# Kernel tuning notes

Hardware: AMD Instinct MI355X
Metric: run time of the kernel (lower is better)

## Reference

```python
import jax, jax.numpy as jnp
import numpy as np

N, K, F, A = 20000, 32, 256, 128
BN_EPS = 1e-3  # Keras BatchNormalization default epsilon


def setup_inputs() -> dict:
    key = jax.random.key(0)
    k1, k2, k3, k4 = jax.random.split(key, 4)
    self_feats = jax.random.normal(k1, (N, F), dtype=jnp.float32)
    neigh_feats = jax.random.normal(k2, (N, K, F), dtype=jnp.float32)
    W_shared = jax.random.normal(k3, (F, A), dtype=jnp.float32) * (1.0 / np.sqrt(F))
    b_shared = jnp.zeros((A,), dtype=jnp.float32)
    gamma = jnp.ones((A,), dtype=jnp.float32)
    beta = jnp.zeros((A,), dtype=jnp.float32)
    W_out = jax.random.normal(k4, (2 * A, 1), dtype=jnp.float32) * (1.0 / np.sqrt(2 * A))
    b_out = jnp.zeros((1,), dtype=jnp.float32)
    return {"self_feats": self_feats, "neigh_feats": neigh_feats,
            "W_shared": W_shared, "b_shared": b_shared,
            "gamma": gamma, "beta": beta, "W_out": W_out, "b_out": b_out}


def _bn_train(x, gamma, beta):
    # BatchNorm in training mode: batch statistics over leading axis
    mean = jnp.mean(x, axis=0, keepdims=True)
    var = jnp.var(x, axis=0, keepdims=True)
    return (x - mean) * jax.lax.rsqrt(var + BN_EPS) * gamma + beta


def reference(self_feats, neigh_feats, W_shared, b_shared, gamma, beta, W_out, b_out):
    # shared Dense + BN on self features: [N, A]
    s = _bn_train(self_feats @ W_shared + b_shared, gamma, beta)
    # shared Dense on neighbor features, BN over flattened [N*K, A] batch
    n = neigh_feats.reshape(-1, F) @ W_shared + b_shared  # [N*K, A]
    n = _bn_train(n, gamma, beta).reshape(neigh_feats.shape[0], neigh_feats.shape[1], -1)  # [N, K, A]
    # broadcast self feats over neighbors and concat: [N, K, 2A]
    s_b = jnp.broadcast_to(s[:, None, :], n.shape)
    concat = jnp.concatenate([s_b, n], axis=2)
    # attention logits: Dense(2A -> 1), activation, softmax over neighbors
    logits = concat @ W_out + b_out  # [N, K, 1]
    logits = jax.nn.relu(logits)
    coeff = jax.nn.softmax(jnp.squeeze(logits, axis=2), axis=-1)  # [N, K]
    return coeff[:, :, None]  # [N, K, 1]
```

## Files before the change

kernel.cpp:

```cpp
#include <hip/hip_runtime.h>
#include <cstdint>
#include <cstddef>


typedef __attribute__((ext_vector_type(8))) short short8;
typedef __attribute__((ext_vector_type(4))) float float4v;

__device__ __forceinline__ unsigned short f2bf(float f) {
  union { float f; unsigned u; } v; v.f = f;
  unsigned r = v.u + 0x7FFFu + ((v.u >> 16) & 1u);
  return (unsigned short)(r >> 16);
}
__device__ __forceinline__ float bfu(unsigned v) {
  union { unsigned u; float f; } t; t.u = v << 16; return t.f;
}
__device__ __forceinline__ unsigned pkbf(float x, float y) {
  return (unsigned)f2bf(x) | ((unsigned)f2bf(y) << 16);
}

__global__ __launch_bounds__(256) void transpose_w(const float* __restrict__ W,
                                                   unsigned short* __restrict__ Wt) {
  const int n = blockIdx.x;
  const int k = threadIdx.x;
  Wt[n * 256 + k] = f2bf(W[k * 128 + n]);
}

#define BROW 264

template <bool GUARD>
__global__ __launch_bounds__(256) void stats_gemm2(
    const float* __restrict__ X, int R, int nTiles,
    const unsigned short* __restrict__ Wt,
    unsigned short* __restrict__ U,
    float* __restrict__ partials) {
  __shared__ __align__(16) unsigned short Bs[128 * BROW];
  __shared__ float cred[1024];

  const int tid  = threadIdx.x;
  const int lane = tid & 63;
  const int wv   = tid >> 6;
  const int quad = lane >> 4;
  const int l16  = lane & 15;

#pragma unroll
  for (int it = 0; it < 16; ++it) {
    int e = it * 256 + tid;
    int r = e >> 5, c = e & 31;
    *(uint4*)&Bs[r * BROW + c * 8] = *(const uint4*)(Wt + r * 256 + c * 8);
  }
  __syncthreads();

  float rs[8], rq[8];
#pragma unroll
  for (int cb = 0; cb < 8; ++cb) { rs[cb] = 0.f; rq[cb] = 0.f; }

  for (int t = blockIdx.x; t < nTiles; t += gridDim.x) {
    const int row0 = t * 128 + wv * 32;
    float4v acc[2][8];
#pragma unroll
    for (int rb = 0; rb < 2; ++rb)
#pragma unroll
      for (int cb = 0; cb < 8; ++cb)
        acc[rb][cb] = (float4v){0.f, 0.f, 0.f, 0.f};

#pragma unroll
    for (int kc = 0; kc < 8; ++kc) {
      short8 a[2];
#pragma unroll
      for (int rb = 0; rb < 2; ++rb) {
        const int gr = row0 + rb * 16 + l16;
        float4 v0 = make_float4(0.f, 0.f, 0.f, 0.f);
        float4 v1 = make_float4(0.f, 0.f, 0.f, 0.f);
        if (!GUARD || gr < R) {
          const float* p = X + (size_t)gr * 256 + kc * 32 + quad * 8;
          v0 = *(const float4*)p;
          v1 = *(const float4*)(p + 4);
        }
        union { short8 s; unsigned u[4]; } af;
        af.u[0] = pkbf(v0.x, v0.y);
        af.u[1] = pkbf(v0.z, v0.w);
        af.u[2] = pkbf(v1.x, v1.y);
        af.u[3] = pkbf(v1.z, v1.w);
        a[rb] = af.s;
      }
#pragma unroll
      for (int cb = 0; cb < 8; ++cb) {
        short8 b = *(const short8*)&Bs[(cb * 16 + l16) * BROW + kc * 32 + quad * 8];
#pragma unroll
        for (int rb = 0; rb < 2; ++rb)
          acc[rb][cb] = __builtin_amdgcn_mfma_f32_16x16x32_bf16(
              a[rb], b, acc[rb][cb], 0, 0, 0);
      }
    }

#pragma unroll
    for (int rb = 0; rb < 2; ++rb) {
#pragma unroll
      for (int cb = 0; cb < 8; ++cb) {
        const int col = cb * 16 + l16;
#pragma unroll
        for (int rg = 0; rg < 4; ++rg) {
          const int grow = row0 + rb * 16 + quad * 4 + rg;
          const float x = acc[rb][cb][rg];
          if (!GUARD || grow < R) U[(size_t)grow * 128 + col] = f2bf(x);
          rs[cb] += x;
          rq[cb] = fmaf(x, x, rq[cb]);
        }
      }
    }
  }

#pragma unroll
  for (int cb = 0; cb < 8; ++cb) {
    float s = rs[cb], q = rq[cb];
    s += __shfl_xor(s, 16); s += __shfl_xor(s, 32);
    q += __shfl_xor(q, 16); q += __shfl_xor(q, 32);
    if (quad == 0) {
      cred[wv * 128 + cb * 16 + l16] = s;
      cred[512 + wv * 128 + cb * 16 + l16] = q;
    }
  }
  __syncthreads();
  float out = 0.f;
  if (tid < 128) {
#pragma unroll
    for (int w = 0; w < 4; ++w) out += cred[w * 128 + tid];
  } else {
#pragma unroll
    for (int w = 0; w < 4; ++w) out += cred[512 + w * 128 + (tid - 128)];
  }
  partials[(size_t)blockIdx.x * 256 + tid] = out;
}

__global__ __launch_bounds__(256) void reduce_partials(
    const float* __restrict__ ps, int ns, const float* __restrict__ pn, int nn,
    float* __restrict__ stats) {
  __shared__ float buf[256];
  const int c = blockIdx.x;
  const int tid = threadIdx.x;
  float a = 0.f;
  for (int g = tid; g < ns; g += 256) a += ps[(size_t)g * 256 + c];
  buf[tid] = a;
  __syncthreads();
  for (int s = 128; s > 0; s >>= 1) {
    if (tid < s) buf[tid] += buf[tid + s];
    __syncthreads();
  }
  if (tid == 0) stats[c] = buf[0];
  float b = 0.f;
  for (int g = tid; g < nn; g += 256) b += pn[(size_t)g * 256 + c];
  __syncthreads();
  buf[tid] = b;
  __syncthreads();
  for (int s = 128; s > 0; s >>= 1) {
    if (tid < s) buf[tid] += buf[tid + s];
    __syncthreads();
  }
  if (tid == 0) stats[256 + c] = buf[0];
}

__global__ __launch_bounds__(128) void setup_kernel(
    const float* __restrict__ stats,
    const float* __restrict__ gamma, const float* __restrict__ beta,
    const float* __restrict__ Wout, const float* __restrict__ bout,
    float* __restrict__ G1, float* __restrict__ G2, float* __restrict__ Cout) {
  __shared__ float carr[128];
  const int tid = threadIdx.x;
  const float invNs = 1.f / 20000.f, invNn = 1.f / 640000.f;
  float ms = stats[tid] * invNs;
  float vs = stats[128 + tid] * invNs - ms * ms;
  float is = rsqrtf(vs + 1e-3f);
  float mn = stats[256 + tid] * invNn;
  float vn = stats[384 + tid] * invNn - mn * mn;
  float in_ = rsqrtf(vn + 1e-3f);
  float w1 = Wout[tid], w2 = Wout[128 + tid];
  float g1 = is * gamma[tid] * w1;
  float g2 = in_ * gamma[tid] * w2;
  G1[tid] = g1;
  G2[tid] = g2;
  carr[tid] = beta[tid] * (w1 + w2) - ms * g1 - mn * g2;
  __syncthreads();
  if (tid == 0) {
    float c = bout[0];
    for (int a = 0; a < 128; ++a) c += carr[a];
    Cout[0] = c;
  }
}

__global__ __launch_bounds__(256) void attn_final(
    const unsigned short* __restrict__ Us,
    const unsigned short* __restrict__ Un,
    const float* __restrict__ G1, const float* __restrict__ G2,
    const float* __restrict__ Cptr, float* __restrict__ out) {
  const int lane = threadIdx.x & 63;
  const int wv = threadIdx.x >> 6;
  const int i = blockIdx.x * 4 + wv;
  const int l16 = lane & 15;
  const int l32 = lane & 31;
  const int quarter = lane >> 4;
  const float C = Cptr[0];

  unsigned su = *(const unsigned*)(Us + (size_t)i * 128 + lane * 2);
  float2 g1p = *(const float2*)(G1 + lane * 2);
  float sd = fmaf(g1p.x, bfu(su), g1p.y * bfu(su >> 16));
#pragma unroll
  for (int m = 32; m >= 1; m >>= 1) sd += __shfl_xor(sd, m);

  const float4 ga = *(const float4*)(G2 + l16 * 8);
  const float4 gb = *(const float4*)(G2 + l16 * 8 + 4);
  const unsigned short* un = Un + (size_t)i * 4096;
  float ml = 0.f;
#pragma unroll
  for (int j = 0; j < 8; ++j) {
    const int nb = j * 4 + quarter;
    uint4 q = *(const uint4*)(un + nb * 128 + l16 * 8);
    float p;
    p = fmaf(ga.x, bfu(q.x), ga.y * bfu(q.x >> 16));
    p = fmaf(ga.z, bfu(q.y), p); p = fmaf(ga.w, bfu(q.y >> 16), p);
    p = fmaf(gb.x, bfu(q.z), p); p = fmaf(gb.y, bfu(q.z >> 16), p);
    p = fmaf(gb.z, bfu(q.w), p); p = fmaf(gb.w, bfu(q.w >> 16), p);
#pragma unroll
    for (int m = 1; m <= 8; m <<= 1) p += __shfl_xor(p, m);
    float s16 = __shfl_xor(p, 16);
    float s32 = __shfl_xor(p, 32);
    float s48 = __shfl_xor(s16, 32);
    if ((l32 >> 2) == j) {
      int x = (l32 & 3) ^ quarter;
      ml = (x == 0) ? p : (x == 1) ? s16 : (x == 2) ? s32 : s48;
    }
  }
  float logit = fmaxf(ml + sd + C, 0.f);
  float mx = logit;
#pragma unroll
  for (int m = 16; m >= 1; m >>= 1) mx = fmaxf(mx, __shfl_xor(mx, m));
  float e = __expf(logit - mx);
  float ssum = e;
#pragma unroll
  for (int m = 16; m >= 1; m >>= 1) ssum += __shfl_xor(ssum, m);
  if (lane < 32) out[(size_t)i * 32 + lane] = e / ssum;
}

extern "C" void kernel_launch(void* const* d_in, const int* in_sizes, int n_in,
                              void* d_out, int out_size, void* d_ws, size_t ws_size,
                              hipStream_t stream) {
  const float* self  = (const float*)d_in[0];
  const float* neigh = (const float*)d_in[1];
  const float* W     = (const float*)d_in[2];
  const float* gamma = (const float*)d_in[4];
  const float* beta  = (const float*)d_in[5];
  const float* Wout  = (const float*)d_in[6];
  const float* bout  = (const float*)d_in[7];
  float* out = (float*)d_out;

  char* ws = (char*)d_ws;
  unsigned short* Wt = (unsigned short*)ws;
  unsigned short* Us = (unsigned short*)(ws + (1 << 16));
  unsigned short* Un = Us + (size_t)20000 * 128;
  float* part_s = (float*)(Un + (size_t)640000 * 128);
  float* part_n = part_s + 157 * 256;
  float* stats  = part_n + 1024 * 256;
  float* G1     = stats + 512;
  float* G2     = G1 + 128;
  float* Cc     = G2 + 128;

  hipLaunchKernelGGL(transpose_w, dim3(128), dim3(256), 0, stream, W, Wt);
  hipLaunchKernelGGL((stats_gemm2<true>), dim3(157), dim3(256), 0, stream,
                     self, 20000, 157, Wt, Us, part_s);
  hipLaunchKernelGGL((stats_gemm2<false>), dim3(1000), dim3(256), 0, stream,
                     neigh, 640000, 5000, Wt, Un, part_n);
  hipLaunchKernelGGL(reduce_partials, dim3(256), dim3(256), 0, stream,
                     part_s, 157, part_n, 1000, stats);
  hipLaunchKernelGGL(setup_kernel, dim3(1), dim3(128), 0, stream,
                     stats, gamma, beta, Wout, bout, G1, G2, Cc);
  hipLaunchKernelGGL(attn_final, dim3(5000), dim3(256), 0, stream,
                     Us, Un, G1, G2, Cc, out);
}
```

Baseline: 1.010 ms.

## Fuse weight transpose, self/neighbor GEMMs and setup into fewer kernels

Merges the self and neighbor stats GEMMs into one launch with block ranges split by input, and converts and transposes W into shared memory inside each block instead of running a separate transpose kernel. Also folds the BN/output-weight setup into attn_final, where each block recomputes G1, G2 and C in shared memory. This removes three launches and their serialization gaps. In exchange every block redoes the W conversion with scattered 2-byte LDS stores, and every attn_final block redoes the small setup computation.

```diff
diff --git a/kernel.cpp b/kernel.cpp
--- a/kernel.cpp
+++ b/kernel.cpp
@@ -18,21 +18,15 @@
   return (unsigned)f2bf(x) | ((unsigned)f2bf(y) << 16);
 }
 
-__global__ __launch_bounds__(256) void transpose_w(const float* __restrict__ W,
-                                                   unsigned short* __restrict__ Wt) {
-  const int n = blockIdx.x;
-  const int k = threadIdx.x;
-  Wt[n * 256 + k] = f2bf(W[k * 128 + n]);
-}
-
 #define BROW 264
-
-template <bool GUARD>
-__global__ __launch_bounds__(256) void stats_gemm2(
-    const float* __restrict__ X, int R, int nTiles,
-    const unsigned short* __restrict__ Wt,
-    unsigned short* __restrict__ U,
-    float* __restrict__ partials) {
+#define NBLK_N 1000
+#define NBLK_S 157
+
+__global__ __launch_bounds__(256) void fused_stats(
+    const float* __restrict__ Xn, const float* __restrict__ Xs,
+    const float* __restrict__ W,
+    unsigned short* __restrict__ Un, unsigned short* __restrict__ Us,
+    float* __restrict__ part_n, float* __restrict__ part_s) {
   __shared__ __align__(16) unsigned short Bs[128 * BROW];
   __shared__ float cred[1024];
 
@@ -42,11 +36,26 @@
   const int quad = lane >> 4;
   const int l16  = lane & 15;
 
-#pragma unroll
-  for (int it = 0; it < 16; ++it) {
+  const float* X; unsigned short* U; float* P;
+  int R, t0, tStride, nT; bool guard;
+  if (blockIdx.x < NBLK_N) {
+    X = Xn; U = Un; P = part_n + (size_t)blockIdx.x * 256;
+    R = 640000; t0 = blockIdx.x; tStride = NBLK_N; nT = 5000; guard = false;
+  } else {
+    int b = blockIdx.x - NBLK_N;
+    X = Xs; U = Us; P = part_s + (size_t)b * 256;
+    R = 20000; t0 = b; tStride = NBLK_S; nT = NBLK_S; guard = true;
+  }
+
+#pragma unroll
+  for (int it = 0; it < 32; ++it) {
     int e = it * 256 + tid;
-    int r = e >> 5, c = e & 31;
-    *(uint4*)&Bs[r * BROW + c * 8] = *(const uint4*)(Wt + r * 256 + c * 8);
+    int k = e >> 5, ng = e & 31;
+    float4 w = *(const float4*)(W + k * 128 + ng * 4);
+    Bs[(ng * 4 + 0) * BROW + k] = f2bf(w.x);
+    Bs[(ng * 4 + 1) * BROW + k] = f2bf(w.y);
+    Bs[(ng * 4 + 2) * BROW + k] = f2bf(w.z);
+    Bs[(ng * 4 + 3) * BROW + k] = f2bf(w.w);
   }
   __syncthreads();
 
@@ -54,8 +63,12 @@
 #pragma unroll
   for (int cb = 0; cb < 8; ++cb) { rs[cb] = 0.f; rq[cb] = 0.f; }
 
-  for (int t = blockIdx.x; t < nTiles; t += gridDim.x) {
+  for (int t = t0; t < nT; t += tStride) {
     const int row0 = t * 128 + wv * 32;
+    bool ok[2];
+    ok[0] = !guard || (row0 + 0 * 16 + l16) < R;
+    ok[1] = !guard || (row0 + 1 * 16 + l16) < R;
+
     float4v acc[2][8];
 #pragma unroll
     for (int rb = 0; rb < 2; ++rb)
@@ -71,7 +84,7 @@
         const int gr = row0 + rb * 16 + l16;
         float4 v0 = make_float4(0.f, 0.f, 0.f, 0.f);
         float4 v1 = make_float4(0.f, 0.f, 0.f, 0.f);
-        if (!GUARD || gr < R) {
+        if (ok[rb]) {
           const float* p = X + (size_t)gr * 256 + kc * 32 + quad * 8;
           v0 = *(const float4*)p;
           v1 = *(const float4*)(p + 4);
@@ -102,7 +115,7 @@
         for (int rg = 0; rg < 4; ++rg) {
           const int grow = row0 + rb * 16 + quad * 4 + rg;
           const float x = acc[rb][cb][rg];
-          if (!GUARD || grow < R) U[(size_t)grow * 128 + col] = f2bf(x);
+          if (!guard || grow < R) U[(size_t)grow * 128 + col] = f2bf(x);
           rs[cb] += x;
           rq[cb] = fmaf(x, x, rq[cb]);
         }
@@ -129,7 +142,7 @@
 #pragma unroll
     for (int w = 0; w < 4; ++w) out += cred[512 + w * 128 + (tid - 128)];
   }
-  partials[(size_t)blockIdx.x * 256 + tid] = out;
+  P[tid] = out;
 }
 
 __global__ __launch_bounds__(256) void reduce_partials(
@@ -159,55 +172,59 @@
   if (tid == 0) stats[256 + c] = buf[0];
 }
 
-__global__ __launch_bounds__(128) void setup_kernel(
+__global__ __launch_bounds__(256) void attn_final(
+    const unsigned short* __restrict__ Us,
+    const unsigned short* __restrict__ Un,
     const float* __restrict__ stats,
     const float* __restrict__ gamma, const float* __restrict__ beta,
     const float* __restrict__ Wout, const float* __restrict__ bout,
-    float* __restrict__ G1, float* __restrict__ G2, float* __restrict__ Cout) {
-  __shared__ float carr[128];
+    float* __restrict__ out) {
+  __shared__ __align__(16) float sG1[128];
+  __shared__ __align__(16) float sG2[128];
+  __shared__ float sCarr[128];
+  __shared__ float sC;
+
   const int tid = threadIdx.x;
-  const float invNs = 1.f / 20000.f, invNn = 1.f / 640000.f;
-  float ms = stats[tid] * invNs;
-  float vs = stats[128 + tid] * invNs - ms * ms;
-  float is = rsqrtf(vs + 1e-3f);
-  float mn = stats[256 + tid] * invNn;
-  float vn = stats[384 + tid] * invNn - mn * mn;
-  float in_ = rsqrtf(vn + 1e-3f);
-  float w1 = Wout[tid], w2 = Wout[128 + tid];
-  float g1 = is * gamma[tid] * w1;
-  float g2 = in_ * gamma[tid] * w2;
-  G1[tid] = g1;
-  G2[tid] = g2;
-  carr[tid] = beta[tid] * (w1 + w2) - ms * g1 - mn * g2;
-  __syncthreads();
-  if (tid == 0) {
-    float c = bout[0];
-    for (int a = 0; a < 128; ++a) c += carr[a];
-    Cout[0] = c;
-  }
-}
-
-__global__ __launch_bounds__(256) void attn_final(
-    const unsigned short* __restrict__ Us,
-    const unsigned short* __restrict__ Un,
-    const float* __restrict__ G1, const float* __restrict__ G2,
-    const float* __restrict__ Cptr, float* __restrict__ out) {
-  const int lane = threadIdx.x & 63;
-  const int wv = threadIdx.x >> 6;
+  if (tid < 128) {
+    const float invNs = 1.f / 20000.f, invNn = 1.f / 640000.f;
+    float ms = stats[tid] * invNs;
+    float vs = stats[128 + tid] * invNs - ms * ms;
+    float is = rsqrtf(vs + 1e-3f);
+    float mn = stats[256 + tid] * invNn;
+    float vn = stats[384 + tid] * invNn - mn * mn;
+    float in_ = rsqrtf(vn + 1e-3f);
+    float w1 = Wout[tid], w2 = Wout[128 + tid];
+    float g1 = is * gamma[tid] * w1;
+    float g2 = in_ * gamma[tid] * w2;
+    sG1[tid] = g1;
+    sG2[tid] = g2;
+    sCarr[tid] = beta[tid] * (w1 + w2) - ms * g1 - mn * g2;
+  }
+  __syncthreads();
+  if (tid < 64) {
+    float c = sCarr[tid] + sCarr[tid + 64];
+#pragma unroll
+    for (int m = 32; m >= 1; m >>= 1) c += __shfl_xor(c, m);
+    if (tid == 0) sC = c + bout[0];
+  }
+  __syncthreads();
+
+  const int lane = tid & 63;
+  const int wv = tid >> 6;
   const int i = blockIdx.x * 4 + wv;
   const int l16 = lane & 15;
   const int l32 = lane & 31;
   const int quarter = lane >> 4;
-  const float C = Cptr[0];
+  const float C = sC;
 
   unsigned su = *(const unsigned*)(Us + (size_t)i * 128 + lane * 2);
-  float2 g1p = *(const float2*)(G1 + lane * 2);
+  float2 g1p = *(const float2*)(sG1 + lane * 2);
   float sd = fmaf(g1p.x, bfu(su), g1p.y * bfu(su >> 16));
 #pragma unroll
   for (int m = 32; m >= 1; m >>= 1) sd += __shfl_xor(sd, m);
 
-  const float4 ga = *(const float4*)(G2 + l16 * 8);
-  const float4 gb = *(const float4*)(G2 + l16 * 8 + 4);
+  const float4 ga = *(const float4*)(sG2 + l16 * 8);
+  const float4 gb = *(const float4*)(sG2 + l16 * 8 + 4);
   const unsigned short* un = Un + (size_t)i * 4096;
   float ml = 0.f;
 #pragma unroll
@@ -253,25 +270,16 @@
   float* out = (float*)d_out;
 
   char* ws = (char*)d_ws;
-  unsigned short* Wt = (unsigned short*)ws;
-  unsigned short* Us = (unsigned short*)(ws + (1 << 16));
+  unsigned short* Us = (unsigned short*)ws;
   unsigned short* Un = Us + (size_t)20000 * 128;
   float* part_s = (float*)(Un + (size_t)640000 * 128);
-  float* part_n = part_s + 157 * 256;
-  float* stats  = part_n + 1024 * 256;
-  float* G1     = stats + 512;
-  float* G2     = G1 + 128;
-  float* Cc     = G2 + 128;
-
-  hipLaunchKernelGGL(transpose_w, dim3(128), dim3(256), 0, stream, W, Wt);
-  hipLaunchKernelGGL((stats_gemm2<true>), dim3(157), dim3(256), 0, stream,
-                     self, 20000, 157, Wt, Us, part_s);
-  hipLaunchKernelGGL((stats_gemm2<false>), dim3(1000), dim3(256), 0, stream,
-                     neigh, 640000, 5000, Wt, Un, part_n);
+  float* part_n = part_s + NBLK_S * 256;
+  float* stats  = part_n + NBLK_N * 256;
+
+  hipLaunchKernelGGL(fused_stats, dim3(NBLK_N + NBLK_S), dim3(256), 0, stream,
+                     neigh, self, W, Un, Us, part_n, part_s);
   hipLaunchKernelGGL(reduce_partials, dim3(256), dim3(256), 0, stream,
-                     part_s, 157, part_n, 1000, stats);
-  hipLaunchKernelGGL(setup_kernel, dim3(1), dim3(128), 0, stream,
-                     stats, gamma, beta, Wout, bout, G1, G2, Cc);
+                     part_s, NBLK_S, part_n, NBLK_N, stats);
   hipLaunchKernelGGL(attn_final, dim3(5000), dim3(256), 0, stream,
-                     Us, Un, G1, G2, Cc, out);
-}
+                     Us, Un, stats, gamma, beta, Wout, bout, out);
+}
```

Measured after the change: 983.9 us. 2.6% less time.
